# Optimization experiments

Hardware: AMD Instinct MI355X
Metric: run time of the kernel (lower is better)

## Reference

```python
import jax, jax.numpy as jnp
import numpy as np

B, DC, DB, DF = 16384, 2048, 768, 256
NF = DB  # num_features (isSwinT=True)
EPS = 1e-5


def setup_inputs() -> dict:
    key = jax.random.key(0)
    ks = jax.random.split(key, 20)
    s = 0.02
    return {
        'x_context': jax.random.normal(ks[0], (B, DC), jnp.float32),
        'x_body': jax.random.normal(ks[1], (B, DB), jnp.float32),
        'x_face': jax.random.normal(ks[2], (B, DF), jnp.float32),
        'Wc': jax.random.normal(ks[3], (NF, DC), jnp.float32) * s,
        'bc': jax.random.normal(ks[4], (NF,), jnp.float32) * s,
        'Wa1': jax.random.normal(ks[5], (128, NF), jnp.float32) * s,
        'ba1': jax.random.normal(ks[6], (128,), jnp.float32) * s,
        'ga': jnp.ones((128,), jnp.float32),
        'bba': jnp.zeros((128,), jnp.float32),
        'Wa2': jax.random.normal(ks[7], (1, 128), jnp.float32) * s,
        'ba2': jax.random.normal(ks[8], (1,), jnp.float32) * s,
        'W1': jax.random.normal(ks[9], (256, NF * 3), jnp.float32) * s,
        'b1': jax.random.normal(ks[10], (256,), jnp.float32) * s,
        'g1': jnp.ones((256,), jnp.float32),
        'be1': jnp.zeros((256,), jnp.float32),
        'Wcat': jax.random.normal(ks[11], (26, 256), jnp.float32) * s,
        'bcat': jax.random.normal(ks[12], (26,), jnp.float32) * s,
    }


def _bn(x, g, b):
    # BatchNorm1d, training mode (biased batch stats), deterministic
    m = jnp.mean(x, axis=0)
    v = jnp.mean((x - m) ** 2, axis=0)
    return (x - m) * jax.lax.rsqrt(v + EPS) * g + b


def reference(x_context, x_body, x_face, Wc, bc, Wa1, ba1, ga, bba, Wa2, ba2,
              W1, b1, g1, be1, Wcat, bcat):
    # face repeated elementwise to body width: [B,256,1]->repeat(3)->view[B,768]
    face = jnp.repeat(x_face, DB // DF, axis=1)              # [B, NF]
    ctx = x_context @ Wc.T + bc                              # [B, NF]
    body = x_body                                            # [B, NF]

    def cross_atten(a, u, v):
        # two 1x1 dot-products, softmax over size-2 dim, weighted sum
        d = jnp.stack([jnp.sum(a * u, axis=1), jnp.sum(a * v, axis=1)], axis=1)  # [B,2]
        att = jax.nn.softmax(d, axis=1)
        # sum over dim2 of a[:, :, None] @ att[:, None, :] == a * att.sum(1)
        return a * jnp.sum(att, axis=1, keepdims=True)

    cfeat = cross_atten(ctx, body, face)
    bfeat = cross_atten(body, ctx, face)
    ffeat = cross_atten(face, ctx, body)

    def fc_att(x):
        h = _bn(x @ Wa1.T + ba1, ga, bba)
        h = jax.nn.gelu(h, approximate=False)
        return h @ Wa2.T + ba2                               # [B, 1]

    score = jax.nn.softmax(
        jnp.concatenate([fc_att(cfeat), fc_att(bfeat), fc_att(ffeat)], axis=1), axis=1)  # [B,3]
    cfeat = cfeat * score[:, 0:1]
    bfeat = bfeat * score[:, 1:2]
    ffeat = ffeat * score[:, 2:3]

    fuse = jnp.concatenate([cfeat, bfeat, ffeat], axis=1) @ W1.T + b1  # [B,256]
    fuse = jax.nn.relu(_bn(fuse, g1, be1))  # dropout p=0.5 treated as identity (eval)
    return fuse @ Wcat.T + bcat             # [B,26]
```

## Files before the change

### kernel.cpp

```cpp
#include <hip/hip_runtime.h>
#include <hip/hip_bf16.h>
#include <stdint.h>

typedef float f32x4 __attribute__((ext_vector_type(4)));
typedef short bf16x8 __attribute__((ext_vector_type(8)));
typedef unsigned short u16;

static constexpr int kB  = 16384;
static constexpr int kDC = 2048;
static constexpr int kNF = 768;
static constexpr float kEps = 1e-5f;

static constexpr size_t OFF_FEATS  = 0;
static constexpr size_t OFF_X      = 75497472;
static constexpr size_t OFF_WCBF   = OFF_X + 67108864;
static constexpr size_t OFF_WA1BF  = OFF_WCBF + 3145728;
static constexpr size_t OFF_W1BF   = OFF_WA1BF + 196608;
static constexpr size_t OFF_FUSE   = OFF_W1BF + 1179648;
static constexpr size_t OFF_SCORES = OFF_FUSE + 16777216;
static constexpr size_t OFF_STATS  = OFF_SCORES + 196608;

static __device__ __forceinline__ u16 f2bf(float x) {
  union { float f; unsigned u; } c; c.f = x;
  unsigned r = c.u + 0x7fffu + ((c.u >> 16) & 1u);
  return (u16)(r >> 16);
}

static __device__ __forceinline__ unsigned pk2(float lo, float hi) {
  union { __hip_bfloat162 h; unsigned u; } c;
  c.h = __float22bfloat162_rn(make_float2(lo, hi));
  return c.u;
}

static __device__ __forceinline__ void cvt4(const float* __restrict__ in, u16* __restrict__ out, long v) {
  const float4 f = ((const float4*)in)[v];
  ((ushort4*)out)[v] = make_ushort4(f2bf(f.x), f2bf(f.y), f2bf(f.z), f2bf(f.w));
}

__global__ __launch_bounds__(256) void prep_kernel(
    const float* __restrict__ xb, const float* __restrict__ xf,
    const float* __restrict__ Wc, const float* __restrict__ Wa1, const float* __restrict__ W1,
    u16* __restrict__ feats, u16* __restrict__ wcbf, u16* __restrict__ wa1bf, u16* __restrict__ w1bf)
{
  const int b = blockIdx.x, t = threadIdx.x;
  if (b < 3072) {
    const long base = (long)b * 1024 + t;
    u16* o = feats + (size_t)kB * kNF;
#pragma unroll
    for (int i = 0; i < 4; ++i) cvt4(xb, o, base + i * 256);
  } else if (b < 4096) {
    const long base = (long)(b - 3072) * 1024 + t;
#pragma unroll
    for (int i = 0; i < 4; ++i) {
      const long v = base + i * 256;
      const float4 f = ((const float4*)xf)[v];
      u16 e0 = f2bf(f.x), e1 = f2bf(f.y), e2 = f2bf(f.z), e3 = f2bf(f.w);
      size_t p = (size_t)v * 4;
      size_t row = p >> 8;
      int col = (int)(p & 255);
      u16* o = feats + (size_t)2 * kB * kNF + row * kNF + col * 3;
      ushort4* o4 = (ushort4*)o;
      o4[0] = make_ushort4(e0, e0, e0, e1);
      o4[1] = make_ushort4(e1, e1, e2, e2);
      o4[2] = make_ushort4(e2, e3, e3, e3);
    }
  } else if (b < 4480) {
    const long base = (long)(b - 4096) * 1024 + t;
#pragma unroll
    for (int i = 0; i < 4; ++i) cvt4(Wc, wcbf, base + i * 256);
  } else if (b < 4504) {
    const long base = (long)(b - 4480) * 1024 + t;
#pragma unroll
    for (int i = 0; i < 4; ++i) cvt4(Wa1, wa1bf, base + i * 256);
  } else {
    const long base = (long)(b - 4504) * 1024 + t;
#pragma unroll
    for (int i = 0; i < 4; ++i) cvt4(W1, w1bf, base + i * 256);
  }
}

static __device__ __forceinline__ void gload16(const void* g, void* l) {
  __builtin_amdgcn_global_load_lds(
      (const __attribute__((address_space(1))) void*)g,
      (__attribute__((address_space(3))) void*)l, 16, 0, 0);
}

__global__ __launch_bounds__(256) void gemm_a32(
    const float* __restrict__ A, const u16* __restrict__ B,
    const float* __restrict__ bias, u16* __restrict__ C)
{
  __shared__ __align__(16) u16 As[128 * 32];
  __shared__ __align__(16) u16 Bs[128 * 32];
  const int bx = blockIdx.x, by = blockIdx.y;
  const size_t m0 = (size_t)bx * 128;
  const int n0 = by * 128;
  const int t = threadIdx.x;
  const int lane = t & 63, wave = t >> 6;
  const int wm = (wave >> 1) * 64, wn = (wave & 1) * 64;
  const int fr = lane & 15, fq = lane >> 4;

  const int srow = t >> 2, scol = (t & 3) * 8;
  const u16* gb0 = B + (size_t)(n0 + srow) * kDC + scol;
  const u16* gb1 = B + (size_t)(n0 + 64 + srow) * kDC + scol;
  u16* lb = Bs + t * 8;

  const int arow = t >> 1, acol = (t & 1) * 16;
  const float* ga = A + (m0 + arow) * (size_t)kDC + acol;
  u16* lawr = As + arow * 32 + acol;

  const u16* fa = As + (wm + fr) * 32 + fq * 8;
  const u16* fb = Bs + (wn + fr) * 32 + fq * 8;

  f32x4 acc[4][4] = {};
  float4 ra0 = ((const float4*)ga)[0], ra1 = ((const float4*)ga)[1],
         ra2 = ((const float4*)ga)[2], ra3 = ((const float4*)ga)[3];

  for (int k = 0; k < 64; ++k) {
    __syncthreads();
    gload16(gb0, lb);
    gload16(gb1, lb + 2048);
    gb0 += 32; gb1 += 32;
    uint4 w0, w1;
    w0.x = pk2(ra0.x, ra0.y); w0.y = pk2(ra0.z, ra0.w);
    w0.z = pk2(ra1.x, ra1.y); w0.w = pk2(ra1.z, ra1.w);
    w1.x = pk2(ra2.x, ra2.y); w1.y = pk2(ra2.z, ra2.w);
    w1.z = pk2(ra3.x, ra3.y); w1.w = pk2(ra3.z, ra3.w);
    ((uint4*)lawr)[0] = w0;
    ((uint4*)(lawr + 8))[0] = w1;
    if (k < 63) {
      ga += 32;
      ra0 = ((const float4*)ga)[0]; ra1 = ((const float4*)ga)[1];
      ra2 = ((const float4*)ga)[2]; ra3 = ((const float4*)ga)[3];
    }
    __syncthreads();
    bf16x8 av[4], bv[4];
#pragma unroll
    for (int mf = 0; mf < 4; ++mf) av[mf] = *(const bf16x8*)(fa + mf * 512);
#pragma unroll
    for (int nf = 0; nf < 4; ++nf) bv[nf] = *(const bf16x8*)(fb + nf * 512);
#pragma unroll
    for (int mf = 0; mf < 4; ++mf)
#pragma unroll
      for (int nf = 0; nf < 4; ++nf)
        acc[mf][nf] = __builtin_amdgcn_mfma_f32_16x16x32_bf16(av[mf], bv[nf], acc[mf][nf], 0, 0, 0);
  }

#pragma unroll
  for (int mf = 0; mf < 4; ++mf) {
    const size_t rb = m0 + wm + mf * 16 + fq * 4;
#pragma unroll
    for (int nf = 0; nf < 4; ++nf) {
      const int gn = n0 + wn + nf * 16 + fr;
      const float bb = bias[gn];
#pragma unroll
      for (int rr = 0; rr < 4; ++rr)
        C[(rb + rr) * (size_t)kNF + gn] = f2bf(acc[mf][nf][rr] + bb);
    }
  }
}

template <int STATS>
__global__ __launch_bounds__(256) void gemm_bt64(
    const u16* __restrict__ A, int lda, const u16* __restrict__ B, int ldb,
    const float* __restrict__ bias, float* __restrict__ C, int ldc, int K,
    float* __restrict__ stats)
{
  __shared__ __align__(16) u16 As[64 * 32];
  __shared__ __align__(16) u16 Bs[128 * 32];
  const int bx = blockIdx.x, by = blockIdx.y;
  const size_t m0 = (size_t)bx * 64;
  const int n0 = by * 128;
  const int t = threadIdx.x;
  const int lane = t & 63, wave = t >> 6;
  const int wn = wave * 32;
  const int fr = lane & 15, fq = lane >> 4;

  const int srow = t >> 2, scol = (t & 3) * 8;
  const u16* ga0 = A + (m0 + srow) * (size_t)lda + scol;
  const u16* gb0 = B + (size_t)(n0 + srow) * ldb + scol;
  const u16* gb1 = B + (size_t)(n0 + 64 + srow) * ldb + scol;
  u16* la = As + t * 8;
  u16* lb = Bs + t * 8;
  const u16* fa = As + fr * 32 + fq * 8;
  const u16* fb = Bs + (wn + fr) * 32 + fq * 8;

  f32x4 acc[4][2] = {};

  const int kt = K >> 5;
  for (int k = 0; k < kt; ++k) {
    __syncthreads();
    gload16(ga0, la);
    gload16(gb0, lb);
    gload16(gb1, lb + 2048);
    ga0 += 32; gb0 += 32; gb1 += 32;
    __syncthreads();
    bf16x8 av[4], bv[2];
#pragma unroll
    for (int mf = 0; mf < 4; ++mf) av[mf] = *(const bf16x8*)(fa + mf * 512);
#pragma unroll
    for (int nf = 0; nf < 2; ++nf) bv[nf] = *(const bf16x8*)(fb + nf * 512);
#pragma unroll
    for (int mf = 0; mf < 4; ++mf)
#pragma unroll
      for (int nf = 0; nf < 2; ++nf)
        acc[mf][nf] = __builtin_amdgcn_mfma_f32_16x16x32_bf16(av[mf], bv[nf], acc[mf][nf], 0, 0, 0);
  }

  float cs[2] = {}, cs2[2] = {};
#pragma unroll
  for (int mf = 0; mf < 4; ++mf) {
    const size_t rb = m0 + mf * 16 + fq * 4;
#pragma unroll
    for (int nf = 0; nf < 2; ++nf) {
      const int gn = n0 + wn + nf * 16 + fr;
      const float bb = bias[gn];
#pragma unroll
      for (int rr = 0; rr < 4; ++rr) {
        const float vv = acc[mf][nf][rr] + bb;
        C[(rb + rr) * (size_t)ldc + gn] = vv;
        if (STATS) { cs[nf] += vv; cs2[nf] += vv * vv; }
      }
    }
  }
  if (STATS) {
    const int f = (int)(m0 >> 14);
#pragma unroll
    for (int nf = 0; nf < 2; ++nf) {
      float s = cs[nf], s2 = cs2[nf];
      s += __shfl_down(s, 32); s2 += __shfl_down(s2, 32);
      s += __shfl_down(s, 16); s2 += __shfl_down(s2, 16);
      if (fq == 0) {
        const int gn = n0 + wn + nf * 16 + fr;
        atomicAdd(&stats[(f * 128 + gn) * 2 + 0], s);
        atomicAdd(&stats[(f * 128 + gn) * 2 + 1], s2);
      }
    }
  }
}

__global__ __launch_bounds__(256) void gemm_fuse64(
    const u16* __restrict__ feats, const u16* __restrict__ w1,
    const float* __restrict__ scores, const float* __restrict__ b1,
    float* __restrict__ fuse, float* __restrict__ fstats)
{
  __shared__ __align__(16) u16 As[64 * 32];
  __shared__ __align__(16) u16 Bs[128 * 32];
  const int bx = blockIdx.x, by = blockIdx.y;
  const size_t m0 = (size_t)bx * 64;
  const int n0 = by * 128;
  const int t = threadIdx.x;
  const int lane = t & 63, wave = t >> 6;
  const int wn = wave * 32;
  const int fr = lane & 15, fq = lane >> 4;
  const int srow = t >> 2, scol = (t & 3) * 8;
  u16* la = As + t * 8;
  u16* lb = Bs + t * 8;
  const u16* fa = As + fr * 32 + fq * 8;
  const u16* fb = Bs + (wn + fr) * 32 + fq * 8;

  f32x4 tot[4][2] = {};

  for (int f = 0; f < 3; ++f) {
    const u16* ga0 = feats + (size_t)f * kB * kNF + (m0 + srow) * (size_t)kNF + scol;
    const u16* gb0 = w1 + f * kNF + (size_t)(n0 + srow) * (3 * kNF) + scol;
    const u16* gb1 = gb0 + (size_t)64 * (3 * kNF);

    f32x4 acc[4][2] = {};
    for (int k = 0; k < (kNF >> 5); ++k) {
      __syncthreads();
      gload16(ga0, la);
      gload16(gb0, lb);
      gload16(gb1, lb + 2048);
      ga0 += 32; gb0 += 32; gb1 += 32;
      __syncthreads();
      bf16x8 av[4], bv[2];
#pragma unroll
      for (int mf = 0; mf < 4; ++mf) av[mf] = *(const bf16x8*)(fa + mf * 512);
#pragma unroll
      for (int nf = 0; nf < 2; ++nf) bv[nf] = *(const bf16x8*)(fb + nf * 512);
#pragma unroll
      for (int mf = 0; mf < 4; ++mf)
#pragma unroll
        for (int nf = 0; nf < 2; ++nf)
          acc[mf][nf] = __builtin_amdgcn_mfma_f32_16x16x32_bf16(av[mf], bv[nf], acc[mf][nf], 0, 0, 0);
    }
#pragma unroll
    for (int mf = 0; mf < 4; ++mf) {
      const size_t rb = m0 + mf * 16 + fq * 4;
#pragma unroll
      for (int rr = 0; rr < 4; ++rr) {
        const float sv = scores[(rb + rr) * 3 + f];
#pragma unroll
        for (int nf = 0; nf < 2; ++nf) tot[mf][nf][rr] += sv * acc[mf][nf][rr];
      }
    }
  }

  float cs[2] = {}, cs2[2] = {};
#pragma unroll
  for (int mf = 0; mf < 4; ++mf) {
    const size_t rb = m0 + mf * 16 + fq * 4;
#pragma unroll
    for (int nf = 0; nf < 2; ++nf) {
      const int gn = n0 + wn + nf * 16 + fr;
      const float bb = b1[gn];
#pragma unroll
      for (int rr = 0; rr < 4; ++rr) {
        const float vv = tot[mf][nf][rr] + bb;
        fuse[(rb + rr) * 256 + gn] = vv;
        cs[nf] += vv; cs2[nf] += vv * vv;
      }
    }
  }
#pragma unroll
  for (int nf = 0; nf < 2; ++nf) {
    float s = cs[nf], s2 = cs2[nf];
    s += __shfl_down(s, 32); s2 += __shfl_down(s2, 32);
    s += __shfl_down(s, 16); s2 += __shfl_down(s2, 16);
    if (fq == 0) {
      const int gn = n0 + wn + nf * 16 + fr;
      atomicAdd(&fstats[gn * 2 + 0], s);
      atomicAdd(&fstats[gn * 2 + 1], s2);
    }
  }
}

__global__ __launch_bounds__(64) void att_kernel(
    const float* __restrict__ H, const float* __restrict__ stats,
    const float* __restrict__ ga, const float* __restrict__ bba,
    const float* __restrict__ Wa2, const float* __restrict__ ba2,
    float* __restrict__ scores)
{
  const int i = blockIdx.x, l = threadIdx.x;
  float d[3];
#pragma unroll
  for (int f = 0; f < 3; ++f) {
    float part = 0.f;
#pragma unroll
    for (int h = 0; h < 2; ++h) {
      const int c = l + h * 64;
      const float sum = stats[(f * 128 + c) * 2 + 0];
      const float sq  = stats[(f * 128 + c) * 2 + 1];
      const float m = sum * (1.f / kB);
      const float var = sq * (1.f / kB) - m * m;
      const float rs = rsqrtf(var + kEps);
      const float x = H[((size_t)f * kB + i) * 128 + c];
      const float xn = (x - m) * rs * ga[c] + bba[c];
      const float ge = 0.5f * xn * (1.f + erff(xn * 0.70710678118f));
      part += ge * Wa2[c];
    }
#pragma unroll
    for (int off = 32; off > 0; off >>= 1) part += __shfl_down(part, off);
    d[f] = part;
  }
  if (l == 0) {
    const float b2 = ba2[0];
    float d0 = d[0] + b2, d1 = d[1] + b2, d2 = d[2] + b2;
    const float mx = fmaxf(d0, fmaxf(d1, d2));
    const float e0 = expf(d0 - mx), e1 = expf(d1 - mx), e2 = expf(d2 - mx);
    const float inv = 1.f / (e0 + e1 + e2);
    scores[i * 3 + 0] = e0 * inv;
    scores[i * 3 + 1] = e1 * inv;
    scores[i * 3 + 2] = e2 * inv;
  }
}

__global__ __launch_bounds__(64) void final_kernel(
    const float* __restrict__ fuse, const float* __restrict__ fstats,
    const float* __restrict__ g1, const float* __restrict__ be1,
    const float* __restrict__ Wcat, const float* __restrict__ bcat,
    float* __restrict__ out)
{
  const int i = blockIdx.x, l = threadIdx.x;
  __shared__ float row[256];
#pragma unroll
  for (int h = 0; h < 4; ++h) {
    const int c = l + h * 64;
    const float sum = fstats[c * 2 + 0], sq = fstats[c * 2 + 1];
    const float m = sum * (1.f / kB);
    const float var = sq * (1.f / kB) - m * m;
    const float rs = rsqrtf(var + kEps);
    const float v = (fuse[(size_t)i * 256 + c] - m) * rs * g1[c] + be1[c];
    row[c] = fmaxf(v, 0.f);
  }
  __syncthreads();
  if (l < 26) {
    float acc = bcat[l];
    const float* w = Wcat + l * 256;
    for (int k2 = 0; k2 < 256; ++k2) acc += row[k2] * w[k2];
    out[(size_t)i * 26 + l] = acc;
  }
}

extern "C" void kernel_launch(void* const* d_in, const int* in_sizes, int n_in,
                              void* d_out, int out_size, void* d_ws, size_t ws_size,
                              hipStream_t stream) {
  (void)in_sizes; (void)n_in; (void)out_size; (void)ws_size;
  const float* xc   = (const float*)d_in[0];
  const float* xb   = (const float*)d_in[1];
  const float* xf   = (const float*)d_in[2];
  const float* Wc   = (const float*)d_in[3];
  const float* bc   = (const float*)d_in[4];
  const float* Wa1  = (const float*)d_in[5];
  const float* ba1  = (const float*)d_in[6];
  const float* ga   = (const float*)d_in[7];
  const float* bba  = (const float*)d_in[8];
  const float* Wa2  = (const float*)d_in[9];
  const float* ba2  = (const float*)d_in[10];
  const float* W1   = (const float*)d_in[11];
  const float* b1   = (const float*)d_in[12];
  const float* g1   = (const float*)d_in[13];
  const float* be1  = (const float*)d_in[14];
  const float* Wcat = (const float*)d_in[15];
  const float* bcat = (const float*)d_in[16];
  float* out = (float*)d_out;

  char* ws = (char*)d_ws;
  u16* feats   = (u16*)(ws + OFF_FEATS);
  float* H     = (float*)(ws + OFF_X);
  u16* wcbf    = (u16*)(ws + OFF_WCBF);
  u16* wa1bf   = (u16*)(ws + OFF_WA1BF);
  u16* w1bf    = (u16*)(ws + OFF_W1BF);
  float* fuse  = (float*)(ws + OFF_FUSE);
  float* scores= (float*)(ws + OFF_SCORES);
  float* hst   = (float*)(ws + OFF_STATS);
  float* fst   = (float*)(ws + OFF_STATS + 3072);

  hipMemsetAsync(ws + OFF_STATS, 0, 5120, stream);
  prep_kernel<<<4648, 256, 0, stream>>>(xb, xf, Wc, Wa1, W1, feats, wcbf, wa1bf, w1bf);
  gemm_a32<<<dim3(128, 6), 256, 0, stream>>>(xc, wcbf, bc, feats);
  gemm_bt64<1><<<dim3(768, 1), 256, 0, stream>>>(feats, kNF, wa1bf, kNF, ba1, H, 128, kNF, hst);
  att_kernel<<<kB, 64, 0, stream>>>(H, hst, ga, bba, Wa2, ba2, scores);
  gemm_fuse64<<<dim3(256, 2), 256, 0, stream>>>(feats, w1bf, scores, b1, fuse, fst);
  final_kernel<<<kB, 64, 0, stream>>>(fuse, fst, g1, be1, Wcat, bcat, out);
}
```

Baseline: 292.2 us.

## Double-buffer LDS tiles in all three GEMM kernels to overlap loads with MFMA

Converts the three GEMM kernels to a two-stage LDS ping-pong. The next K-tile's global-to-LDS loads (and the fp32-to-bf16 conversion of A in gemm_a32) are issued before the current tile's MFMAs, and only one barrier is kept per iteration. The fuse GEMM's three feature loops are flattened into a single 72-step pipeline so prefetching continues across feature boundaries. gemm_a32's A tile is padded to a row stride of 40 to reduce LDS bank conflicts. This doubles LDS use per block, which may lower occupancy.

```diff
diff --git a/kernel.cpp b/kernel.cpp
--- a/kernel.cpp
+++ b/kernel.cpp
@@ -89,8 +89,9 @@
     const float* __restrict__ A, const u16* __restrict__ B,
     const float* __restrict__ bias, u16* __restrict__ C)
 {
-  __shared__ __align__(16) u16 As[128 * 32];
-  __shared__ __align__(16) u16 Bs[128 * 32];
+  constexpr int APAD = 40;
+  __shared__ __align__(16) u16 As[2 * 128 * APAD];
+  __shared__ __align__(16) u16 Bs[2 * 128 * 32];
   const int bx = blockIdx.x, by = blockIdx.y;
   const size_t m0 = (size_t)bx * 128;
   const int n0 = by * 128;
@@ -102,40 +103,51 @@
   const int srow = t >> 2, scol = (t & 3) * 8;
   const u16* gb0 = B + (size_t)(n0 + srow) * kDC + scol;
   const u16* gb1 = B + (size_t)(n0 + 64 + srow) * kDC + scol;
-  u16* lb = Bs + t * 8;
-
-  const int arow = t >> 1, acol = (t & 1) * 16;
-  const float* ga = A + (m0 + arow) * (size_t)kDC + acol;
-  u16* lawr = As + arow * 32 + acol;
-
-  const u16* fa = As + (wm + fr) * 32 + fq * 8;
-  const u16* fb = Bs + (wn + fr) * 32 + fq * 8;
-
-  f32x4 acc[4][4] = {};
-  float4 ra0 = ((const float4*)ga)[0], ra1 = ((const float4*)ga)[1],
-         ra2 = ((const float4*)ga)[2], ra3 = ((const float4*)ga)[3];
-
-  for (int k = 0; k < 64; ++k) {
-    __syncthreads();
-    gload16(gb0, lb);
-    gload16(gb1, lb + 2048);
-    gb0 += 32; gb1 += 32;
+
+  const int arow = t >> 1, ah = (t & 1);
+  const float* ga = A + (m0 + arow) * (size_t)kDC + ah * 16;
+  const int lawoff = arow * APAD + ah * 16;
+
+  float4 ra0, ra1, ra2, ra3;
+  auto loadA = [&]() {
+    ra0 = ((const float4*)ga)[0]; ra1 = ((const float4*)ga)[1];
+    ra2 = ((const float4*)ga)[2]; ra3 = ((const float4*)ga)[3];
+  };
+  auto cvtWrite = [&](u16* dst) {
     uint4 w0, w1;
     w0.x = pk2(ra0.x, ra0.y); w0.y = pk2(ra0.z, ra0.w);
     w0.z = pk2(ra1.x, ra1.y); w0.w = pk2(ra1.z, ra1.w);
     w1.x = pk2(ra2.x, ra2.y); w1.y = pk2(ra2.z, ra2.w);
     w1.z = pk2(ra3.x, ra3.y); w1.w = pk2(ra3.z, ra3.w);
-    ((uint4*)lawr)[0] = w0;
-    ((uint4*)(lawr + 8))[0] = w1;
+    ((uint4*)dst)[0] = w0; ((uint4*)dst)[1] = w1;
+  };
+
+  f32x4 acc[4][4] = {};
+
+  loadA();
+  cvtWrite(As + lawoff);
+  gload16(gb0, Bs + t * 8);
+  gload16(gb1, Bs + t * 8 + 2048);
+  gb0 += 32; gb1 += 32;
+  ga += 32; loadA();
+  __syncthreads();
+
+  for (int k = 0; k < 64; ++k) {
+    const int cur = k & 1;
     if (k < 63) {
-      ga += 32;
-      ra0 = ((const float4*)ga)[0]; ra1 = ((const float4*)ga)[1];
-      ra2 = ((const float4*)ga)[2]; ra3 = ((const float4*)ga)[3];
-    }
-    __syncthreads();
+      u16* an = As + (cur ^ 1) * (128 * APAD);
+      u16* bn = Bs + (cur ^ 1) * (128 * 32);
+      cvtWrite(an + lawoff);
+      gload16(gb0, bn + t * 8);
+      gload16(gb1, bn + t * 8 + 2048);
+      gb0 += 32; gb1 += 32;
+      if (k < 62) { ga += 32; loadA(); }
+    }
+    const u16* fa = As + cur * (128 * APAD) + (wm + fr) * APAD + fq * 8;
+    const u16* fb = Bs + cur * (128 * 32) + (wn + fr) * 32 + fq * 8;
     bf16x8 av[4], bv[4];
 #pragma unroll
-    for (int mf = 0; mf < 4; ++mf) av[mf] = *(const bf16x8*)(fa + mf * 512);
+    for (int mf = 0; mf < 4; ++mf) av[mf] = *(const bf16x8*)(fa + mf * 16 * APAD);
 #pragma unroll
     for (int nf = 0; nf < 4; ++nf) bv[nf] = *(const bf16x8*)(fb + nf * 512);
 #pragma unroll
@@ -143,6 +155,7 @@
 #pragma unroll
       for (int nf = 0; nf < 4; ++nf)
         acc[mf][nf] = __builtin_amdgcn_mfma_f32_16x16x32_bf16(av[mf], bv[nf], acc[mf][nf], 0, 0, 0);
+    __syncthreads();
   }
 
 #pragma unroll
@@ -165,8 +178,8 @@
     const float* __restrict__ bias, float* __restrict__ C, int ldc, int K,
     float* __restrict__ stats)
 {
-  __shared__ __align__(16) u16 As[64 * 32];
-  __shared__ __align__(16) u16 Bs[128 * 32];
+  __shared__ __align__(16) u16 As[2 * 64 * 32];
+  __shared__ __align__(16) u16 Bs[2 * 128 * 32];
   const int bx = blockIdx.x, by = blockIdx.y;
   const size_t m0 = (size_t)bx * 64;
   const int n0 = by * 128;
@@ -179,21 +192,28 @@
   const u16* ga0 = A + (m0 + srow) * (size_t)lda + scol;
   const u16* gb0 = B + (size_t)(n0 + srow) * ldb + scol;
   const u16* gb1 = B + (size_t)(n0 + 64 + srow) * ldb + scol;
-  u16* la = As + t * 8;
-  u16* lb = Bs + t * 8;
-  const u16* fa = As + fr * 32 + fq * 8;
-  const u16* fb = Bs + (wn + fr) * 32 + fq * 8;
 
   f32x4 acc[4][2] = {};
+
+  gload16(ga0, As + t * 8);
+  gload16(gb0, Bs + t * 8);
+  gload16(gb1, Bs + t * 8 + 2048);
+  ga0 += 32; gb0 += 32; gb1 += 32;
+  __syncthreads();
 
   const int kt = K >> 5;
   for (int k = 0; k < kt; ++k) {
-    __syncthreads();
-    gload16(ga0, la);
-    gload16(gb0, lb);
-    gload16(gb1, lb + 2048);
-    ga0 += 32; gb0 += 32; gb1 += 32;
-    __syncthreads();
+    const int cur = k & 1;
+    if (k + 1 < kt) {
+      u16* an = As + (cur ^ 1) * 2048;
+      u16* bn = Bs + (cur ^ 1) * 4096;
+      gload16(ga0, an + t * 8);
+      gload16(gb0, bn + t * 8);
+      gload16(gb1, bn + t * 8 + 2048);
+      ga0 += 32; gb0 += 32; gb1 += 32;
+    }
+    const u16* fa = As + cur * 2048 + fr * 32 + fq * 8;
+    const u16* fb = Bs + cur * 4096 + (wn + fr) * 32 + fq * 8;
     bf16x8 av[4], bv[2];
 #pragma unroll
     for (int mf = 0; mf < 4; ++mf) av[mf] = *(const bf16x8*)(fa + mf * 512);
@@ -204,6 +224,7 @@
 #pragma unroll
       for (int nf = 0; nf < 2; ++nf)
         acc[mf][nf] = __builtin_amdgcn_mfma_f32_16x16x32_bf16(av[mf], bv[nf], acc[mf][nf], 0, 0, 0);
+    __syncthreads();
   }
 
   float cs[2] = {}, cs2[2] = {};
@@ -243,8 +264,8 @@
     const float* __restrict__ scores, const float* __restrict__ b1,
     float* __restrict__ fuse, float* __restrict__ fstats)
 {
-  __shared__ __align__(16) u16 As[64 * 32];
-  __shared__ __align__(16) u16 Bs[128 * 32];
+  __shared__ __align__(16) u16 As[2 * 64 * 32];
+  __shared__ __align__(16) u16 Bs[2 * 128 * 32];
   const int bx = blockIdx.x, by = blockIdx.y;
   const size_t m0 = (size_t)bx * 64;
   const int n0 = by * 128;
@@ -253,47 +274,68 @@
   const int wn = wave * 32;
   const int fr = lane & 15, fq = lane >> 4;
   const int srow = t >> 2, scol = (t & 3) * 8;
-  u16* la = As + t * 8;
-  u16* lb = Bs + t * 8;
-  const u16* fa = As + fr * 32 + fq * 8;
-  const u16* fb = Bs + (wn + fr) * 32 + fq * 8;
-
-  f32x4 tot[4][2] = {};
-
-  for (int f = 0; f < 3; ++f) {
-    const u16* ga0 = feats + (size_t)f * kB * kNF + (m0 + srow) * (size_t)kNF + scol;
-    const u16* gb0 = w1 + f * kNF + (size_t)(n0 + srow) * (3 * kNF) + scol;
-    const u16* gb1 = gb0 + (size_t)64 * (3 * kNF);
-
-    f32x4 acc[4][2] = {};
-    for (int k = 0; k < (kNF >> 5); ++k) {
-      __syncthreads();
-      gload16(ga0, la);
-      gload16(gb0, lb);
-      gload16(gb1, lb + 2048);
-      ga0 += 32; gb0 += 32; gb1 += 32;
-      __syncthreads();
-      bf16x8 av[4], bv[2];
-#pragma unroll
-      for (int mf = 0; mf < 4; ++mf) av[mf] = *(const bf16x8*)(fa + mf * 512);
-#pragma unroll
-      for (int nf = 0; nf < 2; ++nf) bv[nf] = *(const bf16x8*)(fb + nf * 512);
+
+  const u16* ga0; const u16* gb0; const u16* gb1;
+  auto setf = [&](int f) {
+    ga0 = feats + (size_t)f * kB * kNF + (m0 + srow) * (size_t)kNF + scol;
+    gb0 = w1 + f * kNF + (size_t)(n0 + srow) * 2304 + scol;
+    gb1 = gb0 + (size_t)64 * 2304;
+  };
+
+  const f32x4 vzero = {};
+  f32x4 acc[4][2] = {}, tot[4][2] = {};
+
+  setf(0);
+  gload16(ga0, As + t * 8);
+  gload16(gb0, Bs + t * 8);
+  gload16(gb1, Bs + t * 8 + 2048);
+  ga0 += 32; gb0 += 32; gb1 += 32;
+  int pf = 0, pk = 1;
+  int ck = 0, cf = 0;
+  __syncthreads();
+
+  for (int s = 0; s < 72; ++s) {
+    const int cur = s & 1;
+    if (s < 71) {
+      u16* an = As + (cur ^ 1) * 2048;
+      u16* bn = Bs + (cur ^ 1) * 4096;
+      gload16(ga0, an + t * 8);
+      gload16(gb0, bn + t * 8);
+      gload16(gb1, bn + t * 8 + 2048);
+      if (++pk == 24) { pk = 0; ++pf; if (pf < 3) setf(pf); }
+      else { ga0 += 32; gb0 += 32; gb1 += 32; }
+    }
+    const u16* fa = As + cur * 2048 + fr * 32 + fq * 8;
+    const u16* fb = Bs + cur * 4096 + (wn + fr) * 32 + fq * 8;
+    bf16x8 av[4], bv[2];
+#pragma unroll
+    for (int mf = 0; mf < 4; ++mf) av[mf] = *(const bf16x8*)(fa + mf * 512);
+#pragma unroll
+    for (int nf = 0; nf < 2; ++nf) bv[nf] = *(const bf16x8*)(fb + nf * 512);
+#pragma unroll
+    for (int mf = 0; mf < 4; ++mf)
+#pragma unroll
+      for (int nf = 0; nf < 2; ++nf)
+        acc[mf][nf] = __builtin_amdgcn_mfma_f32_16x16x32_bf16(av[mf], bv[nf], acc[mf][nf], 0, 0, 0);
+    if (++ck == 24) {
+      ck = 0;
+#pragma unroll
+      for (int mf = 0; mf < 4; ++mf) {
+        const size_t rb = m0 + mf * 16 + fq * 4;
+#pragma unroll
+        for (int rr = 0; rr < 4; ++rr) {
+          const float sv = scores[(rb + rr) * 3 + cf];
+#pragma unroll
+          for (int nf = 0; nf < 2; ++nf) tot[mf][nf][rr] += sv * acc[mf][nf][rr];
+        }
+      }
 #pragma unroll
       for (int mf = 0; mf < 4; ++mf)
 #pragma unroll
-        for (int nf = 0; nf < 2; ++nf)
-          acc[mf][nf] = __builtin_amdgcn_mfma_f32_16x16x32_bf16(av[mf], bv[nf], acc[mf][nf], 0, 0, 0);
-    }
-#pragma unroll
-    for (int mf = 0; mf < 4; ++mf) {
-      const size_t rb = m0 + mf * 16 + fq * 4;
-#pragma unroll
-      for (int rr = 0; rr < 4; ++rr) {
-        const float sv = scores[(rb + rr) * 3 + f];
-#pragma unroll
-        for (int nf = 0; nf < 2; ++nf) tot[mf][nf][rr] += sv * acc[mf][nf][rr];
-      }
-    }
+        for (int nf = 0; nf < 2; ++nf) acc[mf][nf] = vzero;
+      ++cf;
+    }
+    __syncthreads();
   }
 
   float cs[2] = {}, cs2[2] = {};
```

Result: slower. 299.8 us (+2.6%).
